# Optimization experiments

Measured on AMD Instinct MI355X. Metric: run time of the kernel, lower is better.

## Reference

```python
import jax, jax.numpy as jnp
import numpy as np

TOP_K = 2  # routing_method: renormalize top-2 (topk then softmax over selected logits)


def setup_inputs() -> dict:
    key = jax.random.key(0)
    ks = jax.random.split(key, 5)
    T, H, I, E = 4096, 1024, 4096, 8
    return {
        "hidden_states": jax.random.normal(ks[0], (T, H), jnp.float32),
        "router_logits": jax.random.normal(ks[1], (T, E), jnp.float32),
        "W_gate": jax.random.normal(ks[2], (E, H, I), jnp.float32) * 0.02,  # w1
        "W_up": jax.random.normal(ks[3], (E, H, I), jnp.float32) * 0.02,   # w3
        "W_down": jax.random.normal(ks[4], (E, I, H), jnp.float32) * 0.02, # w2
    }


def reference(hidden_states, router_logits, W_gate, W_up, W_down):
    # Routing: top-k logits, renormalize with softmax over selected logits.
    top_vals, top_idx = jax.lax.top_k(router_logits, TOP_K)        # [T, K]
    routing_weights = jax.nn.softmax(top_vals, axis=-1)            # [T, K]

    E = W_gate.shape[0]
    out = jnp.zeros_like(hidden_states)                            # [T, H]
    for e in range(E):  # fixed small expert loop (structurally distinct weights)
        # combine weight for expert e per token (0 if not routed here)
        w_e = jnp.sum(jnp.where(top_idx == e, routing_weights, 0.0), axis=-1)  # [T]
        gate = hidden_states @ W_gate[e]                           # [T, I]
        up = hidden_states @ W_up[e]                               # [T, I]
        y = (jax.nn.silu(gate) * up) @ W_down[e]                   # [T, H]
        out = out + w_e[:, None] * y
    return out
```

## Files before the change

### kernel.cpp

```cpp
#include <hip/hip_runtime.h>

typedef float    f32x4 __attribute__((ext_vector_type(4)));
typedef _Float16 f16x8 __attribute__((ext_vector_type(8)));
typedef _Float16 f16x4 __attribute__((ext_vector_type(4)));

#define T_TOK 4096
#define HD    1024
#define ID    4096
#define NE    8
#define TOTP  (2*T_TOK)
#define MAXT1 72
#define MAXT2 40

#define WS_CNT   0
#define WS_FILL  64
#define WS_OFF   128
#define WS_TOT   192
#define WS_TOT2  196
#define WS_TEXP  256
#define WS_TM0   (256 + 4*MAXT1)
#define WS_TEXP2 (256 + 8*MAXT1)
#define WS_TM02  (256 + 8*MAXT1 + 4*MAXT2)
#define WS_TOPE  2048
#define WS_TOPW  (WS_TOPE + 4*TOTP)
#define WS_PAIR  (WS_TOPW + 4*TOTP)
#define WS_ACT   ((size_t)1 << 20)
constexpr size_t WS_YBUF = WS_ACT  + 2ull*TOTP*ID;
constexpr size_t WS_HS16 = WS_YBUF + 2ull*TOTP*HD;
constexpr size_t WS_WG16 = WS_HS16 + 2ull*T_TOK*HD;
constexpr size_t WS_WU16 = WS_WG16 + 2ull*NE*HD*ID;
constexpr size_t WS_WD16 = WS_WU16 + 2ull*NE*HD*ID;

__device__ __forceinline__ void gll16(const void* g, void* l) {
  __builtin_amdgcn_global_load_lds(
      (const __attribute__((address_space(1))) unsigned int*)g,
      (__attribute__((address_space(3))) unsigned int*)l, 16, 0, 0);
}

#define WAITV(N) do { \
    asm volatile("s_waitcnt vmcnt(" #N ")" ::: "memory"); \
    __builtin_amdgcn_sched_barrier(0); \
  } while (0)

__device__ __forceinline__ int lofs(int row, int g) {
  return row * 32 + ((g ^ ((row >> 1) & 3)) << 3);
}
__device__ __forceinline__ int lofs64(int row, int g8) {
  return row * 64 + ((g8 ^ (row & 7)) << 3);
}

__global__ void k_router(const float* __restrict__ logits, char* __restrict__ ws) {
  int t = blockIdx.x * blockDim.x + threadIdx.x;
  if (t >= T_TOK) return;
  float v0 = -1e30f, v1 = -1e30f; int i0 = 0, i1 = 0;
  #pragma unroll
  for (int e = 0; e < NE; ++e) {
    float v = logits[t * NE + e];
    if (v > v0)      { v1 = v0; i1 = i0; v0 = v; i0 = e; }
    else if (v > v1) { v1 = v;  i1 = e; }
  }
  float w0 = 1.f / (1.f + __expf(v1 - v0));
  ((int*)(ws + WS_TOPE))[2*t]   = i0;
  ((int*)(ws + WS_TOPE))[2*t+1] = i1;
  ((float*)(ws + WS_TOPW))[2*t]   = w0;
  ((float*)(ws + WS_TOPW))[2*t+1] = 1.f - w0;
  atomicAdd(&((int*)(ws + WS_CNT))[i0], 1);
  atomicAdd(&((int*)(ws + WS_CNT))[i1], 1);
}

__global__ void k_prefix(char* __restrict__ ws) {
  if (threadIdx.x != 0 || blockIdx.x != 0) return;
  const int* cnt = (const int*)(ws + WS_CNT);
  int* off   = (int*)(ws + WS_OFF);
  int* texp  = (int*)(ws + WS_TEXP);
  int* tm0   = (int*)(ws + WS_TM0);
  int* texp2 = (int*)(ws + WS_TEXP2);
  int* tm02  = (int*)(ws + WS_TM02);
  int run = 0, t1 = 0, t2 = 0;
  for (int e = 0; e < NE; ++e) {
    off[e] = run;
    int ne = cnt[e];
    for (int i = 0; i < ne; i += 128) { texp[t1] = e; tm0[t1] = i; ++t1; }
    for (int i = 0; i < ne; i += 256) { texp2[t2] = e; tm02[t2] = i; ++t2; }
    run += ne;
  }
  off[NE] = run;
  *(int*)(ws + WS_TOT)  = t1;
  *(int*)(ws + WS_TOT2) = t2;
}

__global__ void k_scatter(char* __restrict__ ws) {
  int t = blockIdx.x * blockDim.x + threadIdx.x;
  if (t >= T_TOK) return;
  const int* tope = (const int*)(ws + WS_TOPE);
  const int* off  = (const int*)(ws + WS_OFF);
  int* fill = (int*)(ws + WS_FILL);
  int* pair = (int*)(ws + WS_PAIR);
  #pragma unroll
  for (int s = 0; s < 2; ++s) {
    int id = 2*t + s;
    int e = tope[id];
    int pos = off[e] + atomicAdd(&fill[e], 1);
    pair[pos] = id;
  }
}

__global__ void k_hscvt(const float* __restrict__ src, _Float16* __restrict__ dst) {
  int i = blockIdx.x * blockDim.x + threadIdx.x;
  f32x4 v = ((const f32x4*)src)[i];
  f16x4 o;
  #pragma unroll
  for (int j = 0; j < 4; ++j) o[j] = (_Float16)v[j];
  ((f16x4*)dst)[i] = o;
}

__global__ __launch_bounds__(256) void k_wtrans(const float* __restrict__ src,
                                                _Float16* __restrict__ dst,
                                                int K, int N) {
  const int e = blockIdx.z;
  const int n0 = blockIdx.x * 64, k0 = blockIdx.y * 64;
  const float* s = src + (size_t)e * K * N;
  _Float16* d = dst + (size_t)e * (size_t)K * N;
  __shared__ _Float16 t[64][68];
  const int tx = threadIdx.x & 15, ty = threadIdx.x >> 4;
  #pragma unroll
  for (int it = 0; it < 4; ++it) {
    int k = k0 + it*16 + ty;
    f32x4 v = *(const f32x4*)&s[(size_t)k * N + n0 + tx*4];
    #pragma unroll
    for (int j = 0; j < 4; ++j) t[tx*4 + j][it*16 + ty] = (_Float16)v[j];
  }
  __syncthreads();
  #pragma unroll
  for (int it = 0; it < 4; ++it) {
    int n = it*16 + ty;
    *(f16x4*)&d[(size_t)(n0 + n) * K + k0 + tx*4] = *(const f16x4*)&t[n][tx*4];
  }
}

__global__ __launch_bounds__(512, 2) void k_gemm1(
    const _Float16* __restrict__ hs16, const _Float16* __restrict__ WgT,
    const _Float16* __restrict__ WuT, char* __restrict__ ws) {
  const int s = blockIdx.y;
  if (s >= *(const int*)(ws + WS_TOT2)) return;
  const int e    = ((const int*)(ws + WS_TEXP2))[s];
  const int m0   = ((const int*)(ws + WS_TM02))[s];
  const int offE = ((const int*)(ws + WS_OFF))[e];
  const int nE   = ((const int*)(ws + WS_CNT))[e];
  _Float16* __restrict__ act = (_Float16*)(ws + WS_ACT);
  const int n0 = blockIdx.x * 128;
  const int tid = threadIdx.x, lane = tid & 63, wid = tid >> 6;

  __shared__ __align__(16) _Float16 sm[2 * 32768];

  const int r8 = lane >> 3;
  const int q64 = (((lane & 7) ^ r8) << 3);
  const int* __restrict__ pairp = (const int*)(ws + WS_PAIR);
  const _Float16 *aP[4], *gP[2], *uP[2];
  #pragma unroll
  for (int c = 0; c < 4; ++c) {
    int mm = m0 + 32*wid + 8*c + r8;
    int tok = (mm < nE) ? (pairp[offE + mm] >> 1) : 0;
    aP[c] = hs16 + (size_t)tok * HD + q64;
  }
  #pragma unroll
  for (int c = 0; c < 2; ++c) {
    size_t col = (size_t)e * ID + (n0 + 16*wid + 8*c + r8);
    gP[c] = WgT + col * HD + q64;
    uP[c] = WuT + col * HD + q64;
  }

  auto stage8 = [&](int buf, int kt) {
    _Float16* base = sm + buf * 32768;
    const int ko = kt * 64;
    #pragma unroll
    for (int c = 0; c < 4; ++c)
      gll16(aP[c] + ko, base + (32*wid + 8*c) * 64);
    #pragma unroll
    for (int c = 0; c < 2; ++c) {
      gll16(gP[c] + ko, base + 16384 + (16*wid + 8*c) * 64);
      gll16(uP[c] + ko, base + 24576 + (16*wid + 8*c) * 64);
    }
  };

  const int wr = wid >> 2, wc = wid & 3;
  const int l15 = lane & 15, l4 = lane >> 4;
  f32x4 accg[8][2] = {}, accu[8][2] = {};

  auto computeKK = [&](int buf, int kk) {
    const _Float16* b0 = sm + buf * 32768;
    f16x8 afr[8], bg[2], bu[2];
    #pragma unroll
    for (int i = 0; i < 8; ++i) {
      const int row = 128*wr + 16*i + l15;
      afr[i] = *(const f16x8*)&b0[lofs64(row, kk*4 + l4)];
    }
    #pragma unroll
    for (int j = 0; j < 2; ++j) {
      const int row = 32*wc + 16*j + l15;
      bg[j] = *(const f16x8*)&b0[16384 + lofs64(row, kk*4 + l4)];
      bu[j] = *(const f16x8*)&b0[24576 + lofs64(row, kk*4 + l4)];
    }
    __builtin_amdgcn_s_setprio(1);
    #pragma unroll
    for (int i = 0; i < 8; ++i)
      #pragma unroll
      for (int j = 0; j < 2; ++j) {
        accg[i][j] = __builtin_amdgcn_mfma_f32_16x16x32_f16(afr[i], bg[j], accg[i][j], 0, 0, 0);
        accu[i][j] = __builtin_amdgcn_mfma_f32_16x16x32_f16(afr[i], bu[j], accu[i][j], 0, 0, 0);
      }
    __builtin_amdgcn_s_setprio(0);
  };

  const int KT = HD / 64;
  stage8(0, 0);
  WAITV(0);
  __builtin_amdgcn_s_barrier();
  for (int t = 0; t < KT; ++t) {
    const int cur = t & 1;
    if (t + 1 < KT) stage8(cur ^ 1, t + 1);
    computeKK(cur, 0);
    computeKK(cur, 1);
    WAITV(0);
    __builtin_amdgcn_s_barrier();
  }

  #pragma unroll
  for (int i = 0; i < 8; ++i)
    #pragma unroll
    for (int r = 0; r < 4; ++r) {
      const int mm = m0 + 128*wr + 16*i + 4*l4 + r;
      if (mm < nE) {
        const size_t prow = (size_t)(offE + mm) * ID;
        #pragma unroll
        for (int j = 0; j < 2; ++j) {
          float g = accg[i][j][r], u = accu[i][j][r];
          float sv = g / (1.f + __expf(-g)) * u;
          act[prow + n0 + 32*wc + 16*j + l15] = (_Float16)sv;
        }
      }
    }
}

#define G2_BUF 12288
__global__ __launch_bounds__(256, 2) void k_gemm2(const _Float16* __restrict__ WdT,
                                                  char* __restrict__ ws) {
  const int s = blockIdx.y;
  if (s >= *(const int*)(ws + WS_TOT2)) return;
  const int e    = ((const int*)(ws + WS_TEXP2))[s];
  const int m0   = ((const int*)(ws + WS_TM02))[s];
  const int offE = ((const int*)(ws + WS_OFF))[e];
  const int nE   = ((const int*)(ws + WS_CNT))[e];
  const int* __restrict__ pair = (const int*)(ws + WS_PAIR);
  const _Float16* __restrict__ act = (const _Float16*)(ws + WS_ACT);
  _Float16* __restrict__ ybuf = (_Float16*)(ws + WS_YBUF);
  const int n0 = blockIdx.x * 128;
  const int tid = threadIdx.x, lane = tid & 63, wid = tid >> 6;

  __shared__ __align__(16) _Float16 sm[3 * G2_BUF];

  const int rL = lane >> 2;
  const int q  = (((lane & 3) ^ ((lane >> 3) & 3)) << 3);
  const _Float16 *aS[4], *bS[2];
  #pragma unroll
  for (int j = 0; j < 4; ++j) {
    int mm = m0 + 64*wid + 16*j + rL;
    int p = (mm < nE) ? (offE + mm) : offE;
    aS[j] = act + (size_t)p * ID + q;
  }
  #pragma unroll
  for (int j = 0; j < 2; ++j)
    bS[j] = WdT + ((size_t)e * HD + (n0 + 32*wid + 16*j + rL)) * ID + q;

  auto stage = [&](int buf, int kt) {
    _Float16* b = sm + buf * G2_BUF;
    const int ko = kt * 32;
    #pragma unroll
    for (int j = 0; j < 4; ++j) gll16(aS[j] + ko, b + wid*2048 + j*512);
    #pragma unroll
    for (int j = 0; j < 2; ++j) gll16(bS[j] + ko, b + 8192 + wid*1024 + j*512);
  };

  const int wr = wid >> 1, wc = wid & 1;
  const int l15 = lane & 15, l4 = lane >> 4;
  f32x4 acc[8][4] = {};

  auto compute = [&](int buf) {
    const _Float16* b0 = sm + buf * G2_BUF;
    f16x8 afr[8], bfr[4];
    #pragma unroll
    for (int i = 0; i < 8; ++i)
      afr[i] = *(const f16x8*)&b0[lofs(128*wr + 16*i + l15, l4)];
    #pragma unroll
    for (int j = 0; j < 4; ++j)
      bfr[j] = *(const f16x8*)&b0[8192 + lofs(64*wc + 16*j + l15, l4)];
    __builtin_amdgcn_s_setprio(1);
    #pragma unroll
    for (int i = 0; i < 8; ++i)
      #pragma unroll
      for (int j = 0; j < 4; ++j)
        acc[i][j] = __builtin_amdgcn_mfma_f32_16x16x32_f16(afr[i], bfr[j], acc[i][j], 0, 0, 0);
    __builtin_amdgcn_s_setprio(0);
  };

  auto step = [&](int t, int cur, int nb) {
    stage(nb, t + 2);
    WAITV(12);
    __builtin_amdgcn_s_barrier();
    compute(cur);
    __builtin_amdgcn_s_barrier();
  };

  const int KT = ID / 32;
  stage(0, 0); stage(1, 1);
  for (int t = 0; t < KT - 2; t += 3) {
    step(t,     0, 2);
    step(t + 1, 1, 0);
    step(t + 2, 2, 1);
  }
  WAITV(6);
  __builtin_amdgcn_s_barrier();
  compute(0);
  __builtin_amdgcn_s_barrier();
  WAITV(0);
  __builtin_amdgcn_s_barrier();
  compute(1);

  #pragma unroll
  for (int i = 0; i < 8; ++i)
    #pragma unroll
    for (int r = 0; r < 4; ++r) {
      const int mm = m0 + 128*wr + 16*i + 4*l4 + r;
      if (mm < nE) {
        const int id = pair[offE + mm];
        #pragma unroll
        for (int j = 0; j < 4; ++j)
          ybuf[(size_t)id * HD + n0 + 64*wc + 16*j + l15] = (_Float16)acc[i][j][r];
      }
    }
}

__global__ void k_combine(const char* __restrict__ ws, float* __restrict__ out) {
  const int idx = blockIdx.x * blockDim.x + threadIdx.x;
  const int t = idx >> 7, c = idx & 127;
  const float* topw = (const float*)(ws + WS_TOPW);
  const _Float16* yb = (const _Float16*)(ws + WS_YBUF);
  f16x8 y0 = ((const f16x8*)(yb + (size_t)(2*t)     * HD))[c];
  f16x8 y1 = ((const f16x8*)(yb + (size_t)(2*t + 1) * HD))[c];
  const float w0 = topw[2*t], w1 = topw[2*t+1];
  f32x4 o0, o1;
  #pragma unroll
  for (int j = 0; j < 4; ++j) {
    o0[j] = w0 * (float)y0[j]     + w1 * (float)y1[j];
    o1[j] = w0 * (float)y0[4 + j] + w1 * (float)y1[4 + j];
  }
  ((f32x4*)out)[2*idx]     = o0;
  ((f32x4*)out)[2*idx + 1] = o1;
}

extern "C" void kernel_launch(void* const* d_in, const int* in_sizes, int n_in,
                              void* d_out, int out_size, void* d_ws, size_t ws_size,
                              hipStream_t stream) {
  const float* hs     = (const float*)d_in[0];
  const float* logits = (const float*)d_in[1];
  const float* Wg     = (const float*)d_in[2];
  const float* Wu     = (const float*)d_in[3];
  const float* Wd     = (const float*)d_in[4];
  char* ws = (char*)d_ws;

  _Float16* hs16 = (_Float16*)(ws + WS_HS16);
  _Float16* wg16 = (_Float16*)(ws + WS_WG16);
  _Float16* wu16 = (_Float16*)(ws + WS_WU16);
  _Float16* wd16 = (_Float16*)(ws + WS_WD16);

  hipMemsetAsync(ws, 0, 256, stream);
  k_router <<<dim3(T_TOK/256), dim3(256), 0, stream>>>(logits, ws);
  k_prefix <<<dim3(1),         dim3(64),  0, stream>>>(ws);
  k_scatter<<<dim3(T_TOK/256), dim3(256), 0, stream>>>(ws);
  k_hscvt  <<<dim3(T_TOK*HD/4/256), dim3(256), 0, stream>>>(hs, hs16);
  k_wtrans <<<dim3(ID/64, HD/64, NE), dim3(256), 0, stream>>>(Wg, wg16, HD, ID);
  k_wtrans <<<dim3(ID/64, HD/64, NE), dim3(256), 0, stream>>>(Wu, wu16, HD, ID);
  k_wtrans <<<dim3(HD/64, ID/64, NE), dim3(256), 0, stream>>>(Wd, wd16, ID, HD);
  k_gemm1  <<<dim3(ID/128, MAXT2), dim3(512), 0, stream>>>(hs16, wg16, wu16, ws);
  k_gemm2  <<<dim3(HD/128, MAXT2), dim3(256), 0, stream>>>(wd16, ws);
  k_combine<<<dim3(T_TOK*HD/8/256), dim3(256), 0, stream>>>(ws, (float*)d_out);
}
```

Measured before the change: 501.1 us.

## Split-K down-projection GEMM into four slices with larger tiles and combine-side reduction

The down-projection GEMM now splits the K dimension (intermediate size) into four slices along a new grid dimension. Each slice writes fp16 partial outputs into a separate buffer that reuses the gate-weight workspace region. The combine kernel sums the four partials before applying the routing weights. The block also grows to 512 threads with a 256-wide N tile and a double-buffered 64-deep K stage, which raises the block count and gives more parallelism. In exchange, the combine kernel has four times the reads, partials are rounded to fp16 before the sum, and the pipeline is shallower with a full vmcnt wait every iteration.

```diff
diff --git a/kernel.cpp b/kernel.cpp
--- a/kernel.cpp
+++ b/kernel.cpp
@@ -30,6 +30,7 @@
 constexpr size_t WS_WG16 = WS_HS16 + 2ull*T_TOK*HD;
 constexpr size_t WS_WU16 = WS_WG16 + 2ull*NE*HD*ID;
 constexpr size_t WS_WD16 = WS_WU16 + 2ull*NE*HD*ID;
+constexpr size_t WS_YB   = WS_WG16;
 
 __device__ __forceinline__ void gll16(const void* g, void* l) {
   __builtin_amdgcn_global_load_lds(
@@ -42,9 +43,6 @@
     __builtin_amdgcn_sched_barrier(0); \
   } while (0)
 
-__device__ __forceinline__ int lofs(int row, int g) {
-  return row * 32 + ((g ^ ((row >> 1) & 3)) << 3);
-}
 __device__ __forceinline__ int lofs64(int row, int g8) {
   return row * 64 + ((g8 ^ (row & 7)) << 3);
 }
@@ -242,8 +240,7 @@
     }
 }
 
-#define G2_BUF 12288
-__global__ __launch_bounds__(256, 2) void k_gemm2(const _Float16* __restrict__ WdT,
+__global__ __launch_bounds__(512, 2) void k_gemm2(const _Float16* __restrict__ WdT,
                                                   char* __restrict__ ws) {
   const int s = blockIdx.y;
   if (s >= *(const int*)(ws + WS_TOT2)) return;
@@ -251,49 +248,53 @@
   const int m0   = ((const int*)(ws + WS_TM02))[s];
   const int offE = ((const int*)(ws + WS_OFF))[e];
   const int nE   = ((const int*)(ws + WS_CNT))[e];
+  const int h    = blockIdx.z;
+  const int kbase = h * (ID / 4);
   const int* __restrict__ pair = (const int*)(ws + WS_PAIR);
   const _Float16* __restrict__ act = (const _Float16*)(ws + WS_ACT);
-  _Float16* __restrict__ ybuf = (_Float16*)(ws + WS_YBUF);
-  const int n0 = blockIdx.x * 128;
+  _Float16* __restrict__ yb = (_Float16*)(ws + WS_YB) + (size_t)h * TOTP * HD;
+  const int n0 = blockIdx.x * 256;
   const int tid = threadIdx.x, lane = tid & 63, wid = tid >> 6;
 
-  __shared__ __align__(16) _Float16 sm[3 * G2_BUF];
-
-  const int rL = lane >> 2;
-  const int q  = (((lane & 3) ^ ((lane >> 3) & 3)) << 3);
-  const _Float16 *aS[4], *bS[2];
-  #pragma unroll
-  for (int j = 0; j < 4; ++j) {
-    int mm = m0 + 64*wid + 16*j + rL;
+  __shared__ __align__(16) _Float16 sm[2 * 32768];
+
+  const int r8 = lane >> 3;
+  const int q64 = (((lane & 7) ^ r8) << 3);
+  const _Float16 *aP[4], *bP[4];
+  #pragma unroll
+  for (int c = 0; c < 4; ++c) {
+    int mm = m0 + 32*wid + 8*c + r8;
     int p = (mm < nE) ? (offE + mm) : offE;
-    aS[j] = act + (size_t)p * ID + q;
-  }
-  #pragma unroll
-  for (int j = 0; j < 2; ++j)
-    bS[j] = WdT + ((size_t)e * HD + (n0 + 32*wid + 16*j + rL)) * ID + q;
-
-  auto stage = [&](int buf, int kt) {
-    _Float16* b = sm + buf * G2_BUF;
-    const int ko = kt * 32;
-    #pragma unroll
-    for (int j = 0; j < 4; ++j) gll16(aS[j] + ko, b + wid*2048 + j*512);
-    #pragma unroll
-    for (int j = 0; j < 2; ++j) gll16(bS[j] + ko, b + 8192 + wid*1024 + j*512);
+    aP[c] = act + (size_t)p * ID + kbase + q64;
+  }
+  #pragma unroll
+  for (int c = 0; c < 4; ++c)
+    bP[c] = WdT + ((size_t)e * HD + (n0 + 32*wid + 8*c + r8)) * ID + kbase + q64;
+
+  auto stage8 = [&](int buf, int kt) {
+    _Float16* base = sm + buf * 32768;
+    const int ko = kt * 64;
+    #pragma unroll
+    for (int c = 0; c < 4; ++c)
+      gll16(aP[c] + ko, base + (32*wid + 8*c) * 64);
+    #pragma unroll
+    for (int c = 0; c < 4; ++c)
+      gll16(bP[c] + ko, base + 16384 + (32*wid + 8*c) * 64);
   };
 
-  const int wr = wid >> 1, wc = wid & 1;
+  const int wr = wid >> 2, wc = wid & 3;
   const int l15 = lane & 15, l4 = lane >> 4;
   f32x4 acc[8][4] = {};
 
-  auto compute = [&](int buf) {
-    const _Float16* b0 = sm + buf * G2_BUF;
+  auto computeKK = [&](int buf, int kk) {
+    const _Float16* b0 = sm + buf * 32768;
     f16x8 afr[8], bfr[4];
     #pragma unroll
     for (int i = 0; i < 8; ++i)
-      afr[i] = *(const f16x8*)&b0[lofs(128*wr + 16*i + l15, l4)];
+      afr[i] = *(const f16x8*)&b0[lofs64(128*wr + 16*i + l15, kk*4 + l4)];
     #pragma unroll
     for (int j = 0; j < 4; ++j)
-      bfr[j] = *(const f16x8*)&b0[8192 + lofs(64*wc + 16*j + l15, l4)];
+      bfr[j] = *(const f16x8*)&b0[16384 + lofs64(64*wc + 16*j + l15, kk*4 + l4)];
     __builtin_amdgcn_s_setprio(1);
     #pragma unroll
     for (int i = 0; i < 8; ++i)
@@ -303,28 +304,18 @@
     __builtin_amdgcn_s_setprio(0);
   };
 
-  auto step = [&](int t, int cur, int nb) {
-    stage(nb, t + 2);
-    WAITV(12);
-    __builtin_amdgcn_s_barrier();
-    compute(cur);
-    __builtin_amdgcn_s_barrier();
-  };
-
-  const int KT = ID / 32;
-  stage(0, 0); stage(1, 1);
-  for (int t = 0; t < KT - 2; t += 3) {
-    step(t,     0, 2);
-    step(t + 1, 1, 0);
-    step(t + 2, 2, 1);
-  }
-  WAITV(6);
-  __builtin_amdgcn_s_barrier();
-  compute(0);
-  __builtin_amdgcn_s_barrier();
+  const int KT = (ID / 4) / 64;
+  stage8(0, 0);
   WAITV(0);
   __builtin_amdgcn_s_barrier();
-  compute(1);
+  for (int t = 0; t < KT; ++t) {
+    const int cur = t & 1;
+    if (t + 1 < KT) stage8(cur ^ 1, t + 1);
+    computeKK(cur, 0);
+    computeKK(cur, 1);
+    WAITV(0);
+    __builtin_amdgcn_s_barrier();
+  }
 
   #pragma unroll
   for (int i = 0; i < 8; ++i)
@@ -335,7 +326,7 @@
         const int id = pair[offE + mm];
         #pragma unroll
         for (int j = 0; j < 4; ++j)
-          ybuf[(size_t)id * HD + n0 + 64*wc + 16*j + l15] = (_Float16)acc[i][j][r];
+          yb[(size_t)id * HD + n0 + 64*wc + 16*j + l15] = (_Float16)acc[i][j][r];
       }
     }
 }
@@ -344,15 +335,22 @@
   const int idx = blockIdx.x * blockDim.x + threadIdx.x;
   const int t = idx >> 7, c = idx & 127;
   const float* topw = (const float*)(ws + WS_TOPW);
-  const _Float16* yb = (const _Float16*)(ws + WS_YBUF);
-  f16x8 y0 = ((const f16x8*)(yb + (size_t)(2*t)     * HD))[c];
-  f16x8 y1 = ((const f16x8*)(yb + (size_t)(2*t + 1) * HD))[c];
+  const _Float16* yb = (const _Float16*)(ws + WS_YB);
+  float s0[8] = {}, s1[8] = {};
+  #pragma unroll
+  for (int h = 0; h < 4; ++h) {
+    const _Float16* p = yb + (size_t)h * TOTP * HD;
+    f16x8 y0 = ((const f16x8*)(p + (size_t)(2*t)     * HD))[c];
+    f16x8 y1 = ((const f16x8*)(p + (size_t)(2*t + 1) * HD))[c];
+    #pragma unroll
+    for (int j = 0; j < 8; ++j) { s0[j] += (float)y0[j]; s1[j] += (float)y1[j]; }
+  }
   const float w0 = topw[2*t], w1 = topw[2*t+1];
   f32x4 o0, o1;
   #pragma unroll
   for (int j = 0; j < 4; ++j) {
-    o0[j] = w0 * (float)y0[j]     + w1 * (float)y1[j];
-    o1[j] = w0 * (float)y0[4 + j] + w1 * (float)y1[4 + j];
+    o0[j] = w0 * s0[j]     + w1 * s1[j];
+    o1[j] = w0 * s0[4 + j] + w1 * s1[4 + j];
   }
   ((f32x4*)out)[2*idx]     = o0;
   ((f32x4*)out)[2*idx + 1] = o1;
@@ -381,7 +379,7 @@
   k_wtrans <<<dim3(ID/64, HD/64, NE), dim3(256), 0, stream>>>(Wg, wg16, HD, ID);
   k_wtrans <<<dim3(ID/64, HD/64, NE), dim3(256), 0, stream>>>(Wu, wu16, HD, ID);
   k_wtrans <<<dim3(HD/64, ID/64, NE), dim3(256), 0, stream>>>(Wd, wd16, ID, HD);
-  k_gemm1  <<<dim3(ID/128, MAXT2), dim3(512), 0, stream>>>(hs16, wg16, wu16, ws);
-  k_gemm2  <<<dim3(HD/128, MAXT2), dim3(256), 0, stream>>>(wd16, ws);
+  k_gemm1  <<<dim3(ID/128, MAXT2),    dim3(512), 0, stream>>>(hs16, wg16, wu16, ws);
+  k_gemm2  <<<dim3(HD/256, MAXT2, 4), dim3(512), 0, stream>>>(wd16, ws);
   k_combine<<<dim3(T_TOK*HD/8/256), dim3(256), 0, stream>>>(ws, (float*)d_out);
 }
```

Result: faster. 479.9 us (-4.2%).
